# Kernel tuning notes

Measured on AMD Instinct MI355X. Metric: run time of the kernel, lower is better.

The kernel has to match this reference:

```python
import jax, jax.numpy as jnp
import numpy as np

NEG_SLOPE = 0.01  # nn.LeakyReLU default

def _leaky(x):
    return jnp.where(x >= 0, x, NEG_SLOPE * x)

def setup_inputs() -> dict:
    key = jax.random.key(0)
    ks = jax.random.split(key, 8)
    in_ch = 64
    B, H, W = 8, 256, 256
    x = jax.random.normal(ks[0], (B, 2 * in_ch, H, W), dtype=jnp.float32)
    dims = [(64, 128), (32, 64), (16, 32), (8, 16), (4, 8), (2, 4), (1, 2)]
    inp = {"x": x}
    for i, (o, c) in enumerate(dims):
        # kaiming_normal_ fan_out, relu: std = sqrt(2 / fan_out), fan_out = o*1*1
        std = np.sqrt(2.0 / o).astype(np.float32)
        inp[f"w{i+1}"] = jax.random.normal(ks[i + 1], (o, c), dtype=jnp.float32) * std
    return inp

def reference(x, w1, w2, w3, w4, w5, w6, w7):
    # Each 1x1 conv (bias-free) is a per-pixel matmul over channels.
    h = x
    for w in (w1, w2, w3, w4, w5, w6):
        h = _leaky(jnp.einsum('bchw,oc->bohw', h, w))
    out = jnp.einsum('bchw,oc->bohw', h, w7)  # final conv, no activation
    return out
```

## Files before the change

kernel.cpp:

```cpp
#include <hip/hip_runtime.h>


#define NEG_SLOPE 0.01f
constexpr int HW = 65536;
constexpr int GRID = 512;
constexpr int TPB  = 8;
constexpr size_t TSTRIDE = (size_t)128 * HW;

typedef __attribute__((ext_vector_type(8))) short bf16x8;
typedef __attribute__((ext_vector_type(4))) float f32x4;
typedef __attribute__((ext_vector_type(2))) float f32x2;

__device__ __forceinline__ float leaky(float v) { return fmaxf(v, v * NEG_SLOPE); }

__device__ __forceinline__ unsigned pk2(float a, float b) {
    __bf16 ba = (__bf16)a, bb = (__bf16)b;
    unsigned short ua = __builtin_bit_cast(unsigned short, ba);
    unsigned short ub = __builtin_bit_cast(unsigned short, bb);
    return (unsigned)ua | ((unsigned)ub << 16);
}

__device__ __forceinline__ bf16x8 loadA(const float* __restrict__ wsrc, int C, int m, int k) {
    f32x4 lo = *(const f32x4*)(wsrc + m * C + k);
    f32x4 hi = *(const f32x4*)(wsrc + m * C + k + 4);
    union { bf16x8 v; unsigned u[4]; } r;
    r.u[0] = pk2(lo[0], lo[1]); r.u[1] = pk2(lo[2], lo[3]);
    r.u[2] = pk2(hi[0], hi[1]); r.u[3] = pk2(hi[2], hi[3]);
    return r.v;
}

__device__ __forceinline__ void async_cp16(const float* g, float* l) {
    __builtin_amdgcn_global_load_lds((const __attribute__((address_space(1))) unsigned*)g,
                                     (__attribute__((address_space(3))) unsigned*)l,
                                     16, 0, 0);
}

__device__ __forceinline__ void cfence() { asm volatile("" ::: "memory"); }

__global__ __launch_bounds__(256, 2) void fused_ring3_kernel(
    const float* __restrict__ x,
    const float* __restrict__ w1, const float* __restrict__ w2,
    const float* __restrict__ w3, const float* __restrict__ w4,
    const float* __restrict__ w5, const float* __restrict__ w6,
    const float* __restrict__ w7, float* __restrict__ out) {
    __shared__ float lds_x[4][3][1024];
    __shared__ float lds_s[4][1088];
    __shared__ float lds_tw[176];

    const int tid = threadIdx.x;
    if (tid < 128)      lds_tw[tid] = w4[tid];
    else if (tid < 160) lds_tw[tid] = w5[tid - 128];
    else if (tid < 168) lds_tw[tid] = w6[tid - 160];
    else if (tid < 170) lds_tw[tid] = w7[tid - 168];

    const int w    = tid >> 6;
    const int lane = tid & 63;
    const int n    = lane & 15;
    const int q    = lane >> 4;
    const int pl   = lane & 31;
    const int r    = lane >> 3;
    const int s4   = (lane & 7) * 4;

    const int b = blockIdx.x;
    const float* xg = x + b * 128 + w * 32;

    __syncthreads();

    bf16x8 a1[4][4];
#pragma unroll
    for (int Mt = 0; Mt < 4; ++Mt)
#pragma unroll
        for (int kc = 0; kc < 4; ++kc)
            a1[Mt][kc] = loadA(w1, 128, Mt * 16 + n, kc * 32 + q * 8);
    bf16x8 a2[2][2];
#pragma unroll
    for (int Mt = 0; Mt < 2; ++Mt)
#pragma unroll
        for (int kc = 0; kc < 2; ++kc)
            a2[Mt][kc] = loadA(w2, 64, Mt * 16 + n, kc * 32 + q * 8);
    bf16x8 a3 = loadA(w3, 32, n, q * 8);
    cfence();
    __builtin_amdgcn_sched_barrier(0);

    float* ldsw = &lds_x[w][0][0];
#define STAGE(BASE, KCX, BUF) do {                                                   \
        const float* gb_ = (BASE) + (size_t)((KCX) * 32 + r) * HW;                   \
        float* lb_ = ldsw + (BUF) * 1024;                                            \
        _Pragma("unroll")                                                            \
        for (int i_ = 0; i_ < 4; ++i_)                                               \
            async_cp16(gb_ + (size_t)(i_ * 8) * HW + (s4 ^ (i_ * 8)), lb_ + i_ * 256); \
    } while (0)

    STAGE(xg, 0, 0);
    STAGE(xg, 1, 1);
    STAGE(xg, 2, 2);
    cfence();

    const int pq = q * 8;
    int bi = 0;

    for (int it = 0; it < TPB; ++it) {
        const float* xg_it = xg + (size_t)it * TSTRIDE;
        const float* xg_nt = xg_it + TSTRIDE;

        f32x4 acc1[4][2];
#pragma unroll
        for (int Mt = 0; Mt < 4; ++Mt)
#pragma unroll
            for (int Nt = 0; Nt < 2; ++Nt) acc1[Mt][Nt] = (f32x4){0.f, 0.f, 0.f, 0.f};

#pragma unroll
        for (int kc = 0; kc < 4; ++kc) {
            if (kc < 2) {
                if (it == 0) asm volatile("s_waitcnt vmcnt(8)" ::: "memory");
                else         asm volatile("s_waitcnt vmcnt(9)" ::: "memory");
            } else if (kc == 2) {
                if (it == 0)            asm volatile("s_waitcnt vmcnt(8)" ::: "memory");
                else if (it == TPB - 1) asm volatile("s_waitcnt vmcnt(5)" ::: "memory");
                else                    asm volatile("s_waitcnt vmcnt(9)" ::: "memory");
            } else {
                if (it == TPB - 1) asm volatile("s_waitcnt vmcnt(0)" ::: "memory");
                else               asm volatile("s_waitcnt vmcnt(8)" ::: "memory");
            }
            __builtin_amdgcn_sched_barrier(0);

            const float* xb = ldsw + bi * 1024;
#pragma unroll
            for (int Nt = 0; Nt < 2; ++Nt) {
                const int pxsw = (Nt * 16 + n) ^ pq;
                float t[8];
#pragma unroll
                for (int j = 0; j < 8; ++j)
                    t[j] = xb[(pq + j) * 32 + pxsw];
                union { bf16x8 v; unsigned u[4]; } bb;
                bb.u[0] = pk2(t[0], t[1]); bb.u[1] = pk2(t[2], t[3]);
                bb.u[2] = pk2(t[4], t[5]); bb.u[3] = pk2(t[6], t[7]);
#pragma unroll
                for (int Mt = 0; Mt < 4; ++Mt)
                    acc1[Mt][Nt] = __builtin_amdgcn_mfma_f32_16x16x32_bf16(a1[Mt][kc], bb.v, acc1[Mt][Nt], 0, 0, 0);
            }
            __builtin_amdgcn_sched_barrier(0);

            if (kc == 0)           STAGE(xg_it, 3, bi);
            else if (it < TPB - 1) STAGE(xg_nt, kc - 1, bi);
            cfence();
            bi = (bi == 2) ? 0 : bi + 1;
        }

        float* Sw = &lds_s[w][0];
        short* h1 = (short*)Sw;
#pragma unroll
        for (int Mt = 0; Mt < 4; ++Mt)
#pragma unroll
            for (int Nt = 0; Nt < 2; ++Nt) {
                int px = Nt * 16 + n;
                uint2 v;
                v.x = pk2(leaky(acc1[Mt][Nt][0]), leaky(acc1[Mt][Nt][1]));
                v.y = pk2(leaky(acc1[Mt][Nt][2]), leaky(acc1[Mt][Nt][3]));
                *(uint2*)(h1 + px * 68 + Mt * 16 + q * 4) = v;
            }
        cfence();

        f32x4 acc2[2][2];
#pragma unroll
        for (int Mt = 0; Mt < 2; ++Mt)
#pragma unroll
            for (int Nt = 0; Nt < 2; ++Nt) acc2[Mt][Nt] = (f32x4){0.f, 0.f, 0.f, 0.f};
#pragma unroll
        for (int Nt = 0; Nt < 2; ++Nt)
#pragma unroll
            for (int kc = 0; kc < 2; ++kc) {
                int off = (Nt * 16 + n) * 68 + kc * 32 + q * 8;
                uint2 lo = *(const uint2*)(h1 + off);
                uint2 hi = *(const uint2*)(h1 + off + 4);
                union { bf16x8 v; unsigned u[4]; } bb;
                bb.u[0] = lo.x; bb.u[1] = lo.y; bb.u[2] = hi.x; bb.u[3] = hi.y;
#pragma unroll
                for (int Mt = 0; Mt < 2; ++Mt)
                    acc2[Mt][Nt] = __builtin_amdgcn_mfma_f32_16x16x32_bf16(a2[Mt][kc], bb.v, acc2[Mt][Nt], 0, 0, 0);
            }
        cfence();

        short* h2 = (short*)Sw;
#pragma unroll
        for (int Mt = 0; Mt < 2; ++Mt)
#pragma unroll
            for (int Nt = 0; Nt < 2; ++Nt) {
                int px = Nt * 16 + n;
                uint2 v;
                v.x = pk2(leaky(acc2[Mt][Nt][0]), leaky(acc2[Mt][Nt][1]));
                v.y = pk2(leaky(acc2[Mt][Nt][2]), leaky(acc2[Mt][Nt][3]));
                *(uint2*)(h2 + px * 36 + Mt * 16 + q * 4) = v;
            }
        cfence();

        f32x4 acc3[2];
#pragma unroll
        for (int Nt = 0; Nt < 2; ++Nt) {
            int off = (Nt * 16 + n) * 36 + q * 8;
            uint2 lo = *(const uint2*)(h2 + off);
            uint2 hi = *(const uint2*)(h2 + off + 4);
            union { bf16x8 v; unsigned u[4]; } bb;
            bb.u[0] = lo.x; bb.u[1] = lo.y; bb.u[2] = hi.x; bb.u[3] = hi.y;
            f32x4 zero = {0.f, 0.f, 0.f, 0.f};
            acc3[Nt] = __builtin_amdgcn_mfma_f32_16x16x32_bf16(a3, bb.v, zero, 0, 0, 0);
        }
        cfence();

        float* h3 = Sw;
#pragma unroll
        for (int Nt = 0; Nt < 2; ++Nt) {
            int px = Nt * 16 + n;
            f32x2 va = {leaky(acc3[Nt][0]), leaky(acc3[Nt][1])};
            f32x2 vb = {leaky(acc3[Nt][2]), leaky(acc3[Nt][3])};
            *(f32x2*)(h3 + px * 18 + q * 4)     = va;
            *(f32x2*)(h3 + px * 18 + q * 4 + 2) = vb;
        }
        cfence();

        float hh[16];
#pragma unroll
        for (int c = 0; c < 16; ++c) hh[c] = h3[pl * 18 + c];

        float g4[8];
#pragma unroll
        for (int o = 0; o < 8; ++o) {
            float a = 0.f;
#pragma unroll
            for (int c = 0; c < 16; ++c) a = fmaf(lds_tw[o * 16 + c], hh[c], a);
            g4[o] = leaky(a);
        }
        float g5[4];
#pragma unroll
        for (int o = 0; o < 4; ++o) {
            float a = 0.f;
#pragma unroll
            for (int c = 0; c < 8; ++c) a = fmaf(lds_tw[128 + o * 8 + c], g4[c], a);
            g5[o] = leaky(a);
        }
        float g6[2];
#pragma unroll
        for (int o = 0; o < 2; ++o) {
            float a = 0.f;
#pragma unroll
            for (int c = 0; c < 4; ++c) a = fmaf(lds_tw[160 + o * 4 + c], g5[c], a);
            g6[o] = leaky(a);
        }
        float res = fmaf(lds_tw[168], g6[0], lds_tw[169] * g6[1]);
        if (lane < 32) out[b * 128 + it * 65536 + w * 32 + pl] = res;
        cfence();
    }
#undef STAGE
}

extern "C" void kernel_launch(void* const* d_in, const int* in_sizes, int n_in,
                              void* d_out, int out_size, void* d_ws, size_t ws_size,
                              hipStream_t stream) {
    const float* x  = (const float*)d_in[0];
    const float* w1 = (const float*)d_in[1];
    const float* w2 = (const float*)d_in[2];
    const float* w3 = (const float*)d_in[3];
    const float* w4 = (const float*)d_in[4];
    const float* w5 = (const float*)d_in[5];
    const float* w6 = (const float*)d_in[6];
    const float* w7 = (const float*)d_in[7];
    float* out = (float*)d_out;

    fused_ring3_kernel<<<GRID, 256, 0, stream>>>(x, w1, w2, w3, w4, w5, w6, w7, out);
}
```

Measured before the change: 381.8 us.

## Spread next-tile prefetches across tail layers and split tail MLP across wave halves

Moves the async global-to-LDS prefetches for the next tile's first three K chunks out of the layer-1 MFMA loop and issues them after each later layer (h1 store, layer 2, layer 3). The wait counts are adjusted to match, so loads overlap the tail computation rather than crowding the main loop. The scalar 16→8→4→2→1 tail is split across the two 32-lane halves of each wave, each doing half the reduction and combining with a cross-half shuffle. This removes the idle upper-half lanes but adds shuffles, and it shortens the prefetch distance for the third chunk, which could expose memory latency.

```diff
diff --git a/kernel.cpp b/kernel.cpp
--- a/kernel.cpp
+++ b/kernel.cpp
@@ -37,7 +37,7 @@
 
 __device__ __forceinline__ void cfence() { asm volatile("" ::: "memory"); }
 
-__global__ __launch_bounds__(256, 2) void fused_ring3_kernel(
+__global__ __launch_bounds__(256, 2) void fused_spread_kernel(
     const float* __restrict__ x,
     const float* __restrict__ w1, const float* __restrict__ w2,
     const float* __restrict__ w3, const float* __restrict__ w4,
@@ -58,6 +58,7 @@
     const int n    = lane & 15;
     const int q    = lane >> 4;
     const int pl   = lane & 31;
+    const int half = lane >> 5;
     const int r    = lane >> 3;
     const int s4   = (lane & 7) * 4;
 
@@ -97,11 +98,16 @@
     cfence();
 
     const int pq = q * 8;
-    int bi = 0;
+    int bt = 0;
 
     for (int it = 0; it < TPB; ++it) {
         const float* xg_it = xg + (size_t)it * TSTRIDE;
         const float* xg_nt = xg_it + TSTRIDE;
+        const bool   more  = (it < TPB - 1);
+
+        int b1 = bt + 1; if (b1 >= 3) b1 -= 3;
+        int b2 = bt + 2; if (b2 >= 3) b2 -= 3;
+        const int bufk[4] = {bt, b1, b2, bt};
 
         f32x4 acc1[4][2];
 #pragma unroll
@@ -111,20 +117,18 @@
 
 #pragma unroll
         for (int kc = 0; kc < 4; ++kc) {
-            if (kc < 2) {
+            if (kc <= 1) {
                 if (it == 0) asm volatile("s_waitcnt vmcnt(8)" ::: "memory");
                 else         asm volatile("s_waitcnt vmcnt(9)" ::: "memory");
             } else if (kc == 2) {
-                if (it == 0)            asm volatile("s_waitcnt vmcnt(8)" ::: "memory");
-                else if (it == TPB - 1) asm volatile("s_waitcnt vmcnt(5)" ::: "memory");
-                else                    asm volatile("s_waitcnt vmcnt(9)" ::: "memory");
+                if (it == 0) asm volatile("s_waitcnt vmcnt(4)" ::: "memory");
+                else         asm volatile("s_waitcnt vmcnt(5)" ::: "memory");
             } else {
-                if (it == TPB - 1) asm volatile("s_waitcnt vmcnt(0)" ::: "memory");
-                else               asm volatile("s_waitcnt vmcnt(8)" ::: "memory");
+                asm volatile("s_waitcnt vmcnt(0)" ::: "memory");
             }
             __builtin_amdgcn_sched_barrier(0);
 
-            const float* xb = ldsw + bi * 1024;
+            const float* xb = ldsw + bufk[kc] * 1024;
 #pragma unroll
             for (int Nt = 0; Nt < 2; ++Nt) {
                 const int pxsw = (Nt * 16 + n) ^ pq;
@@ -141,10 +145,7 @@
             }
             __builtin_amdgcn_sched_barrier(0);
 
-            if (kc == 0)           STAGE(xg_it, 3, bi);
-            else if (it < TPB - 1) STAGE(xg_nt, kc - 1, bi);
-            cfence();
-            bi = (bi == 2) ? 0 : bi + 1;
+            if (kc == 0) { STAGE(xg_it, 3, bt); cfence(); }
         }
 
         float* Sw = &lds_s[w][0];
@@ -160,6 +161,7 @@
                 *(uint2*)(h1 + px * 68 + Mt * 16 + q * 4) = v;
             }
         cfence();
+        if (more) { STAGE(xg_nt, 0, b1); cfence(); }
 
         f32x4 acc2[2][2];
 #pragma unroll
@@ -180,6 +182,7 @@
                     acc2[Mt][Nt] = __builtin_amdgcn_mfma_f32_16x16x32_bf16(a2[Mt][kc], bb.v, acc2[Mt][Nt], 0, 0, 0);
             }
         cfence();
+        if (more) { STAGE(xg_nt, 1, b2); cfence(); }
 
         short* h2 = (short*)Sw;
 #pragma unroll
@@ -217,17 +220,19 @@
             *(f32x2*)(h3 + px * 18 + q * 4 + 2) = vb;
         }
         cfence();
-
-        float hh[16];
-#pragma unroll
-        for (int c = 0; c < 16; ++c) hh[c] = h3[pl * 18 + c];
+        if (more) { STAGE(xg_nt, 2, bt); cfence(); }
+
+        float hh[8];
+#pragma unroll
+        for (int c = 0; c < 8; ++c) hh[c] = h3[pl * 18 + half * 8 + c];
 
         float g4[8];
 #pragma unroll
         for (int o = 0; o < 8; ++o) {
             float a = 0.f;
 #pragma unroll
-            for (int c = 0; c < 16; ++c) a = fmaf(lds_tw[o * 16 + c], hh[c], a);
+            for (int c = 0; c < 8; ++c) a = fmaf(lds_tw[o * 16 + half * 8 + c], hh[c], a);
+            a += __shfl_xor(a, 32, 64);
             g4[o] = leaky(a);
         }
         float g5[4];
@@ -235,20 +240,25 @@
         for (int o = 0; o < 4; ++o) {
             float a = 0.f;
 #pragma unroll
-            for (int c = 0; c < 8; ++c) a = fmaf(lds_tw[128 + o * 8 + c], g4[c], a);
+            for (int c = 0; c < 4; ++c)
+                a = fmaf(lds_tw[128 + o * 8 + half * 4 + c], g4[half * 4 + c], a);
+            a += __shfl_xor(a, 32, 64);
             g5[o] = leaky(a);
         }
         float g6[2];
 #pragma unroll
         for (int o = 0; o < 2; ++o) {
-            float a = 0.f;
-#pragma unroll
-            for (int c = 0; c < 4; ++c) a = fmaf(lds_tw[160 + o * 4 + c], g5[c], a);
+            float a = fmaf(lds_tw[160 + o * 4 + half * 2], g5[half * 2],
+                           lds_tw[160 + o * 4 + half * 2 + 1] * g5[half * 2 + 1]);
+            a += __shfl_xor(a, 32, 64);
             g6[o] = leaky(a);
         }
-        float res = fmaf(lds_tw[168], g6[0], lds_tw[169] * g6[1]);
+        float a7 = lds_tw[168 + half] * g6[half];
+        float res = a7 + __shfl_xor(a7, 32, 64);
         if (lane < 32) out[b * 128 + it * 65536 + w * 32 + pl] = res;
         cfence();
+
+        bt = b1;
     }
 #undef STAGE
 }
@@ -266,5 +276,5 @@
     const float* w7 = (const float*)d_in[7];
     float* out = (float*)d_out;
 
-    fused_ring3_kernel<<<GRID, 256, 0, stream>>>(x, w1, w2, w3, w4, w5, w6, w7, out);
-}
+    fused_spread_kernel<<<GRID, 256, 0, stream>>>(x, w1, w2, w3, w4, w5, w6, w7, out);
+}
```

Result: no change. 378.0 us (-1.0%).
